# Kernel tuning notes

Hardware: AMD Instinct MI355X
Metric: run time of the kernel (lower is better)

The kernel has to match this reference:

```python
import jax, jax.numpy as jnp
import numpy as np

SQRT2PI = float(np.sqrt(2.0 * np.pi))
DN = 20          # disperse_number / heat-map side
OUT_CH = 32      # conv out_channels
MINY, MAXY, SD = 0.0, 50.0, 0.3
BN_EPS = 1e-5


def setup_inputs() -> dict:
    key = jax.random.key(0)
    ks = jax.random.split(key, 8)
    N_ATOM, N_ELE, N_NODE = 65536, 16384, 8192
    oe = jax.random.uniform(ks[0], (N_ATOM, 17), dtype=jnp.float32)
    node_ele_idx = jax.random.randint(ks[1], (N_ELE, 4), 0, N_ATOM, dtype=jnp.int64)
    ele_atom_idx = jax.random.randint(ks[2], (N_NODE, 2), 0, N_ELE, dtype=jnp.int64)
    conv_w = jax.random.normal(ks[3], (OUT_CH, 1, 3, 3), dtype=jnp.float32) * 0.1
    conv_b = jnp.zeros((OUT_CH,), jnp.float32)
    bn_gamma = jnp.ones((OUT_CH,), jnp.float32)
    bn_beta = jnp.zeros((OUT_CH,), jnp.float32)
    w1 = jax.random.normal(ks[4], (500, OUT_CH * DN * DN), dtype=jnp.float32) * 0.01
    b1 = jnp.zeros((500,), jnp.float32)
    w2 = jax.random.normal(ks[5], (60, 500), dtype=jnp.float32) * 0.05
    b2 = jnp.zeros((60,), jnp.float32)
    return dict(oe=oe, node_ele_idx=node_ele_idx, ele_atom_idx=ele_atom_idx,
                conv_w=conv_w, conv_b=conv_b, bn_gamma=bn_gamma, bn_beta=bn_beta,
                w1=w1, b1=b1, w2=w2, b2=b2)


def _distribute(rows):
    # rows: (N_node, 17). Gaussian soft histogram onto DN-point grid per row,
    # per-value max-normalization, masked sum over the 17 values, row max-normalization.
    grid = jnp.linspace(MINY, MAXY, DN).astype(rows.dtype)          # (DN,)
    mask = (rows > 0.0) & (rows < 110.0)                            # filter 0 < y < 110
    pdf = jnp.exp(-(grid[None, None, :] - rows[:, :, None]) ** 2 /
                  (2.0 * SD * SD)) / (SQRT2PI * SD)                 # (N, 17, DN)
    m = jnp.max(pdf, axis=-1, keepdims=True)
    pdf = jnp.where(m != 0, pdf / m, pdf)                           # yi / max(yi)
    pdf = pdf * mask[:, :, None]
    s = jnp.sum(pdf, axis=1)                                        # (N, DN)
    smax = jnp.max(s, axis=-1, keepdims=True)
    return jnp.where(smax != 0, s / smax, s)


def reference(oe, node_ele_idx, ele_atom_idx, conv_w, conv_b,
              bn_gamma, bn_beta, w1, b1, w2, b2):
    # merge_idx(oe, node_ele_idx): gather atoms per element, mean-reduce
    g = jnp.mean(oe[node_ele_idx], axis=1)                          # (N_ele, 17)
    g = g / jnp.linalg.norm(g, axis=1, keepdims=True)
    # merge_idx(..., ele_atom_idx, method='sum')
    h = jnp.sum(g[ele_atom_idx], axis=1)                            # (N_node, 17)
    d = _distribute(h)                                              # (N_node, DN)
    # outer-sum heat map: a[n,i,j] = d[n,j], b[n,i,j] = d[n,i]
    x1 = (d[:, None, :] + d[:, :, None])[:, None, :, :]             # (N_node,1,DN,DN)
    x = jax.lax.conv_general_dilated(
        x1, conv_w, window_strides=(1, 1), padding='SAME',
        dimension_numbers=('NCHW', 'OIHW', 'NCHW')) + conv_b[None, :, None, None]
    # Dropout2d is identity in eval mode. BatchNorm2d: training-mode batch stats.
    mu = jnp.mean(x, axis=(0, 2, 3), keepdims=True)
    var = jnp.var(x, axis=(0, 2, 3), keepdims=True)
    xn = (x - mu) / jnp.sqrt(var + BN_EPS)
    x = xn * bn_gamma[None, :, None, None] + bn_beta[None, :, None, None] + x1
    x = x.reshape(x.shape[0], -1)                                   # (N_node, 32*400)
    x = jax.nn.relu(x @ w1.T + b1)
    x = x @ w2.T + b2
    return x.reshape(x.shape[0], 20, 3)
```

## Files before the change

### kernel.cpp

```cpp
#include <hip/hip_runtime.h>
#include <hip/hip_bf16.h>
#include <math.h>

#define NFEAT 17
#define DN 20
#define OCH 32
#define H1 500
#define H2 60

#define DK 4

#define NPB 256
#define NBW 64

#define OFF_D      0
#define OFF_MOMP   32768
#define OFF_MT     33664
#define OFF_PLAIN  34112
#define OFF_M      36112
#define OFF_RS     100112
#define OFF_U4     116112
#define OFF_CST    118112
#define OFF_W2T    118624

__global__ __launch_bounds__(512) void k_main(const float* __restrict__ oe,
                                              const int* __restrict__ nei,
                                              const int* __restrict__ eai,
                                              const float* __restrict__ w2,
                                              const float* __restrict__ convw,
                                              const float* __restrict__ w1,
                                              float* __restrict__ dmat,
                                              float* __restrict__ momp,
                                              float* __restrict__ w2t,
                                              float* __restrict__ MT,
                                              float* __restrict__ plainU,
                                              float* __restrict__ Mmat,
                                              float* __restrict__ rowsum,
                                              int n_node) {
  __shared__ float smem[19136];
  int tid = threadIdx.x;
  int nbd = (n_node + NPB - 1) / NPB;
  int bx = blockIdx.x;

  if (bx < H1) {
    float* sW    = smem;
    float* rowRS = sW + 13440;
    float* rowRW = rowRS + 640;
    float* colCS = rowRW + 1920;
    float* colCW = colCS + 640;
    float* swq   = colCW + 1920;
    float* swp   = swq + 288;
    if (tid < OCH) {
      int c = tid;
      float w[3][3];
#pragma unroll
      for (int p = 0; p < 3; ++p)
#pragma unroll
        for (int q = 0; q < 3; ++q) w[p][q] = convw[c * 9 + p * 3 + q];
#pragma unroll
      for (int p = 0; p < 3; ++p) {
        swq[(c * 3 + p) * 3 + 0] = w[p][1] + w[p][2];
        swq[(c * 3 + p) * 3 + 1] = w[p][0] + w[p][1] + w[p][2];
        swq[(c * 3 + p) * 3 + 2] = w[p][0] + w[p][1];
      }
#pragma unroll
      for (int q = 0; q < 3; ++q) {
        swp[(c * 3 + q) * 3 + 0] = w[1][q] + w[2][q];
        swp[(c * 3 + q) * 3 + 1] = w[0][q] + w[1][q] + w[2][q];
        swp[(c * 3 + q) * 3 + 2] = w[0][q] + w[1][q];
      }
    }
    __syncthreads();

    const float* wbase = w1 + (size_t)bx * (OCH * DN * DN);
    for (int pair = tid; pair < OCH * DN; pair += 512) {
      int c = pair / DN;
      const float4* r = (const float4*)(wbase + pair * DN);
      float4 v0 = r[0], v1 = r[1], v2 = r[2], v3 = r[3], v4 = r[4];
      float first = v0.x, last = v4.w;
      float rs = v0.x + v0.y + v0.z + v0.w + v1.x + v1.y + v1.z + v1.w +
                 v2.x + v2.y + v2.z + v2.w + v3.x + v3.y + v3.z + v3.w +
                 v4.x + v4.y + v4.z + v4.w;
      float mid = rs - first - last;
#pragma unroll
      for (int p = 0; p < 3; ++p)
        rowRW[p * 640 + pair] = first * swq[(c * 3 + p) * 3 + 0] +
                                mid   * swq[(c * 3 + p) * 3 + 1] +
                                last  * swq[(c * 3 + p) * 3 + 2];
      rowRS[pair] = rs;
      float* dst = &sW[pair * 21];
      dst[0] = v0.x; dst[1] = v0.y; dst[2] = v0.z; dst[3] = v0.w;
      dst[4] = v1.x; dst[5] = v1.y; dst[6] = v1.z; dst[7] = v1.w;
      dst[8] = v2.x; dst[9] = v2.y; dst[10] = v2.z; dst[11] = v2.w;
      dst[12] = v3.x; dst[13] = v3.y; dst[14] = v3.z; dst[15] = v3.w;
      dst[16] = v4.x; dst[17] = v4.y; dst[18] = v4.z; dst[19] = v4.w;
    }
    __syncthreads();
    for (int pair = tid; pair < OCH * DN; pair += 512) {
      int c = pair / DN, j = pair - c * DN;
      const float* src = &sW[c * DN * 21 + j];
      float cs = 0.f, first = 0.f, last = 0.f;
#pragma unroll
      for (int i = 0; i < DN; ++i) {
        float vv = src[i * 21];
        cs += vv;
        if (i == 0) first = vv;
        if (i == DN - 1) last = vv;
      }
      float mid = cs - first - last;
#pragma unroll
      for (int q = 0; q < 3; ++q)
        colCW[q * 640 + pair] = first * swp[(c * 3 + q) * 3 + 0] +
                                mid   * swp[(c * 3 + q) * 3 + 1] +
                                last  * swp[(c * 3 + q) * 3 + 2];
      colCS[pair] = cs;
    }
    __syncthreads();
    if (tid < 128) {
      int c = tid >> 2, a = tid & 3;
      float m = rowRW[640 + c * 20 + a] + colCW[640 + c * 20 + a]
              + rowRW[c * 20 + a + 1]   + colCW[c * 20 + a + 1];
      if (a > 0) m += rowRW[1280 + c * 20 + a - 1] + colCW[1280 + c * 20 + a - 1];
      Mmat[((size_t)bx * OCH + c) * 4 + a] = m;
    } else if (tid >= 128 && tid < 128 + OCH) {
      int c = tid - 128;
      float s = 0.f;
#pragma unroll
      for (int i = 0; i < DN; ++i) s += rowRS[c * 20 + i];
      rowsum[(size_t)bx * OCH + c] = s;
    } else if (tid >= 192 && tid < 192 + DK) {
      int a = tid - 192;
      float s = 0.f;
#pragma unroll
      for (int c = 0; c < OCH; ++c) s += rowRS[c * 20 + a] + colCS[c * 20 + a];
      plainU[bx * DK + a] = s;
    }
    return;
  }

  int rb = bx - H1;
  if (rb < nbd) {
    float* dls = smem;
    int nl = tid >> 1, half = tid & 1;
    int n = rb * NPB + nl;

    float v[NFEAT];
#pragma unroll
    for (int f = 0; f < NFEAT; ++f) v[f] = 0.f;
    if (n < n_node) {
      int e = eai[(size_t)n * 2 + half];
      float a4[NFEAT];
#pragma unroll
      for (int f = 0; f < NFEAT; ++f) a4[f] = 0.f;
#pragma unroll
      for (int m = 0; m < 4; ++m) {
        int at = nei[(size_t)e * 4 + m];
        const float* row = oe + (size_t)at * NFEAT;
#pragma unroll
        for (int f = 0; f < NFEAT; ++f) a4[f] += row[f];
      }
      float nrm = 0.f;
#pragma unroll
      for (int f = 0; f < NFEAT; ++f) { float t = a4[f] * 0.25f; a4[f] = t; nrm += t * t; }
      float inv = 1.0f / sqrtf(nrm);
#pragma unroll
      for (int f = 0; f < NFEAT; ++f) v[f] = a4[f] * inv;
    }
    float h[NFEAT];
#pragma unroll
    for (int f = 0; f < NFEAT; ++f) h[f] = v[f] + __shfl_xor(v[f], 1);

    const float step = 50.0f / 19.0f;
    const float inv2 = 1.0f / (2.0f * 0.3f * 0.3f);
    float s0 = 0.f, s1 = 0.f, s2 = 0.f, s3 = 0.f;
    int f0 = half ? 9 : 0, f1 = half ? NFEAT : 9;
    for (int f = f0; f < f1; ++f) {
      float y = h[f];
      if (!(y > 0.0f && y < 110.0f)) continue;
      float t0 = -y, t1 = step - y, t2 = 2.f * step - y, t3 = 3.f * step - y;
      float e0 = __expf(-t0 * t0 * inv2);
      float e1 = __expf(-t1 * t1 * inv2);
      float e2 = __expf(-t2 * t2 * inv2);
      float e3 = __expf(-t3 * t3 * inv2);
      float mx = fmaxf(fmaxf(e0, e1), fmaxf(e2, e3));
      if (mx > 0.f) {
        float im = 1.0f / mx;
        s0 += e0 * im; s1 += e1 * im; s2 += e2 * im; s3 += e3 * im;
      }
    }
    s0 += __shfl_xor(s0, 1); s1 += __shfl_xor(s1, 1);
    s2 += __shfl_xor(s2, 1); s3 += __shfl_xor(s3, 1);
    float smax = fmaxf(fmaxf(s0, s1), fmaxf(s2, s3));
    float ism = (smax > 0.f) ? 1.0f / smax : 1.0f;
    if (half == 0) {
      float d0 = s0 * ism, d1 = s1 * ism, d2 = s2 * ism, d3 = s3 * ism;
      dls[nl * 5 + 0] = d0; dls[nl * 5 + 1] = d1;
      dls[nl * 5 + 2] = d2; dls[nl * 5 + 3] = d3;
      if (n < n_node)
        *(float4*)(dmat + (size_t)n * DK) = make_float4(d0, d1, d2, d3);
    }
    __syncthreads();
    if (tid < 14) {
      int u = tid;
      float acc = 0.f;
      if (u < 10) {
        int aa = 0, rem = u;
        while (rem >= DK - aa) { rem -= DK - aa; ++aa; }
        int bb = aa + rem;
        for (int l = 0; l < NPB; ++l) acc += dls[l * 5 + aa] * dls[l * 5 + bb];
      } else {
        int aa = u - 10;
        for (int l = 0; l < NPB; ++l) acc += dls[l * 5 + aa];
      }
      momp[(size_t)u * NBW + rb] = acc;
    }
    return;
  }

  int tb = rb - nbd;
  if (tb < 8) {
    float (*sT)[61] = (float(*)[61])smem;
    int o0 = tb * 64;
    int lo = tid & 63, jr = tid >> 6;
    for (int j = jr; j < H2; j += 8)
      if (o0 + lo < H1) sT[lo][j] = w2[(size_t)j * H1 + o0 + lo];
    __syncthreads();
    int jj = tid & 63, orr = tid >> 6;
    for (int ol = orr; ol < 64; ol += 8) {
      int o = o0 + ol;
      if (o < H1) w2t[(size_t)o * 64 + jj] = (jj < H2) ? sT[ol][jj] : 0.f;
    }
    return;
  }

  {
    float* swqL = smem;
    float* swpL = smem + 288;
    float* MTs  = smem + 576;
    if (tid < OCH) {
      int c = tid;
      float w[3][3];
#pragma unroll
      for (int p = 0; p < 3; ++p)
#pragma unroll
        for (int q = 0; q < 3; ++q) w[p][q] = convw[c * 9 + p * 3 + q];
#pragma unroll
      for (int p = 0; p < 3; ++p) {
        swqL[(c * 3 + p) * 3 + 0] = w[p][1] + w[p][2];
        swqL[(c * 3 + p) * 3 + 1] = w[p][0] + w[p][1] + w[p][2];
        swqL[(c * 3 + p) * 3 + 2] = w[p][0] + w[p][1];
      }
#pragma unroll
      for (int q = 0; q < 3; ++q) {
        swpL[(c * 3 + q) * 3 + 0] = w[1][q] + w[2][q];
        swpL[(c * 3 + q) * 3 + 1] = w[0][q] + w[1][q] + w[2][q];
        swpL[(c * 3 + q) * 3 + 2] = w[0][q] + w[1][q];
      }
    }
    for (int idx = tid; idx < OCH * 14; idx += 512) MTs[idx] = 0.f;
    __syncthreads();
    int c = tid & 31, grp = tid >> 5;
    float wqr[3][3], wpr[3][3];
#pragma unroll
    for (int p = 0; p < 3; ++p)
#pragma unroll
      for (int k = 0; k < 3; ++k) {
        wqr[p][k] = swqL[(c * 3 + p) * 3 + k];
        wpr[p][k] = swpL[(c * 3 + p) * 3 + k];
      }
    float T0 = 0, T1 = 0, T2 = 0, T3 = 0;
    float M0 = 0, M1 = 0, M2 = 0, M3 = 0, M4 = 0, M5 = 0, M6 = 0, M7 = 0, M8 = 0, M9 = 0;
    for (int pos = grp; pos < DN * DN; pos += 16) {
      int i = pos / DN, j = pos - (pos / DN) * DN;
      int icls = (i == 0) ? 0 : ((i == DN - 1) ? 2 : 1);
      int jcls = (j == 0) ? 0 : ((j == DN - 1) ? 2 : 1);
      float t0 = 0, t1 = 0, t2 = 0, t3 = 0;
      int p;
      p = 0 - i + 1; if ((unsigned)p <= 2u) t0 += wqr[p][jcls];
      p = 1 - i + 1; if ((unsigned)p <= 2u) t1 += wqr[p][jcls];
      p = 2 - i + 1; if ((unsigned)p <= 2u) t2 += wqr[p][jcls];
      p = 3 - i + 1; if ((unsigned)p <= 2u) t3 += wqr[p][jcls];
      p = 0 - j + 1; if ((unsigned)p <= 2u) t0 += wpr[p][icls];
      p = 1 - j + 1; if ((unsigned)p <= 2u) t1 += wpr[p][icls];
      p = 2 - j + 1; if ((unsigned)p <= 2u) t2 += wpr[p][icls];
      p = 3 - j + 1; if ((unsigned)p <= 2u) t3 += wpr[p][icls];
      T0 += t0; T1 += t1; T2 += t2; T3 += t3;
      M0 += t0 * t0; M1 += t0 * t1; M2 += t0 * t2; M3 += t0 * t3;
      M4 += t1 * t1; M5 += t1 * t2; M6 += t1 * t3;
      M7 += t2 * t2; M8 += t2 * t3; M9 += t3 * t3;
    }
    atomicAdd(&MTs[c * 14 + 0], T0); atomicAdd(&MTs[c * 14 + 1], T1);
    atomicAdd(&MTs[c * 14 + 2], T2); atomicAdd(&MTs[c * 14 + 3], T3);
    atomicAdd(&MTs[c * 14 + 4], M0); atomicAdd(&MTs[c * 14 + 5], M1);
    atomicAdd(&MTs[c * 14 + 6], M2); atomicAdd(&MTs[c * 14 + 7], M3);
    atomicAdd(&MTs[c * 14 + 8], M4); atomicAdd(&MTs[c * 14 + 9], M5);
    atomicAdd(&MTs[c * 14 + 10], M6); atomicAdd(&MTs[c * 14 + 11], M7);
    atomicAdd(&MTs[c * 14 + 12], M8); atomicAdd(&MTs[c * 14 + 13], M9);
    __syncthreads();
    for (int idx = tid; idx < OCH * 14; idx += 512) MT[idx] = MTs[idx];
  }
}

__global__ __launch_bounds__(512) void k_combine(const float* __restrict__ momp,
                                                 const float* __restrict__ MT,
                                                 const float* __restrict__ convb,
                                                 const float* __restrict__ gamma,
                                                 const float* __restrict__ beta,
                                                 const float* __restrict__ b1,
                                                 const float* __restrict__ plainU,
                                                 const float* __restrict__ Mmat,
                                                 const float* __restrict__ rowsum,
                                                 int nbd, int n_node,
                                                 float* __restrict__ U4,
                                                 float* __restrict__ Cst) {
  __shared__ float sac[OCH], scc[OCH], phat[10], S4[4], mred[14];
  int tid = threadIdx.x;
  if (tid < 14) {
    float acc = 0.f;
    const float* mp = momp + (size_t)tid * NBW;
    for (int b = 0; b < nbd; ++b) acc += mp[b];
    mred[tid] = acc;
  }
  __syncthreads();
  if (tid < 14) {
    float vv = mred[tid];
    if (tid < 10) {
      int aa = 0, rem = tid;
      while (rem >= DK - aa) { rem -= DK - aa; ++aa; }
      int bb = aa + rem;
      phat[tid] = (aa == bb ? 1.f : 2.f) * vv;
    } else {
      S4[tid - 10] = vv;
    }
  }
  __syncthreads();
  if (tid < OCH) {
    int c = tid;
    const float* mt = MT + c * 14;
    float q2 = mt[0] * S4[0] + mt[1] * S4[1] + mt[2] * S4[2] + mt[3] * S4[3];
    float q1 = 0.f;
#pragma unroll
    for (int u = 0; u < 10; ++u) q1 += mt[4 + u] * phat[u];
    float b_c = convb[c];
    float Nt = (float)n_node * 400.f;
    float S1 = q2 + Nt * b_c;
    float S2 = q1 + 2.f * b_c * q2 + Nt * b_c * b_c;
    float mu = S1 / Nt;
    float var = S2 / Nt - mu * mu;
    float aa = gamma[c] / sqrtf(var + 1e-5f);
    sac[c] = aa;
    scc[c] = aa * (b_c - mu) + beta[c];
  }
  __syncthreads();

  int o0 = blockIdx.x * 63;
  for (int idx = tid; idx < 63 * DK; idx += 512) {
    int ol = idx >> 2, a = idx & 3;
    int o = o0 + ol;
    if (o < H1) {
      float u = plainU[o * DK + a];
      const float* mrow = Mmat + (size_t)o * (OCH * 4) + a;
#pragma unroll
      for (int c = 0; c < OCH; ++c) u += sac[c] * mrow[c * 4];
      U4[o * DK + a] = u;
    }
  }
  if (tid < 63) {
    int o = o0 + tid;
    if (o < H1) {
      float s = b1[o];
      const float* rr = rowsum + (size_t)o * OCH;
#pragma unroll
      for (int c = 0; c < OCH; ++c) s += scc[c] * rr[c];
      Cst[o] = s;
    }
  }
}

#define NTN 16
__global__ __launch_bounds__(256, 4) void k_final(const float* __restrict__ dmat,
                                                  const float* __restrict__ U4,
                                                  const float* __restrict__ Cst,
                                                  const float* __restrict__ w2t,
                                                  const float* __restrict__ b2,
                                                  float* __restrict__ out, int n_node) {
  __shared__ float h1s[H1][20];
  __shared__ float pacc[4][NTN][64];
  int tid = threadIdx.x;
  int n0 = blockIdx.x * NTN;

  {
    int node = tid & 15, kq = tid >> 4;
    float4 d4 = make_float4(0.f, 0.f, 0.f, 0.f);
    if (n0 + node < n_node)
      d4 = *(const float4*)(dmat + (size_t)(n0 + node) * DK);
    for (int k = kq; k < H1; k += 16) {
      float4 u4 = *(const float4*)(U4 + (size_t)k * DK);
      float z = Cst[k] + u4.x * d4.x + u4.y * d4.y + u4.z * d4.z + u4.w * d4.w;
      h1s[k][node] = fmaxf(z, 0.f);
    }
  }
  __syncthreads();

  {
    int w = tid >> 6;
    int lane = tid & 63;
    int q = lane >> 4;
    int og = lane & 15;
    float a0x = 0.f, a0y = 0.f, a0z = 0.f, a0w = 0.f;
    float a1x = 0.f, a1y = 0.f, a1z = 0.f, a1w = 0.f;
    float a2x = 0.f, a2y = 0.f, a2z = 0.f, a2w = 0.f;
    float a3x = 0.f, a3y = 0.f, a3z = 0.f, a3w = 0.f;
    int k0 = w * 125, k1 = k0 + 125;
    for (int k = k0; k < k1; ++k) {
      float4 hv = *(const float4*)&h1s[k][q * 4];
      float4 wv = *(const float4*)(w2t + (size_t)k * 64 + og * 4);
      a0x += hv.x * wv.x; a0y += hv.x * wv.y; a0z += hv.x * wv.z; a0w += hv.x * wv.w;
      a1x += hv.y * wv.x; a1y += hv.y * wv.y; a1z += hv.y * wv.z; a1w += hv.y * wv.w;
      a2x += hv.z * wv.x; a2y += hv.z * wv.y; a2z += hv.z * wv.z; a2w += hv.z * wv.w;
      a3x += hv.w * wv.x; a3y += hv.w * wv.y; a3z += hv.w * wv.z; a3w += hv.w * wv.w;
    }
    *(float4*)&pacc[w][q * 4 + 0][og * 4] = make_float4(a0x, a0y, a0z, a0w);
    *(float4*)&pacc[w][q * 4 + 1][og * 4] = make_float4(a1x, a1y, a1z, a1w);
    *(float4*)&pacc[w][q * 4 + 2][og * 4] = make_float4(a2x, a2y, a2z, a2w);
    *(float4*)&pacc[w][q * 4 + 3][og * 4] = make_float4(a3x, a3y, a3z, a3w);
  }
  __syncthreads();

  for (int idx = tid; idx < NTN * H2; idx += 256) {
    int n = idx / H2, o = idx - n * H2;
    float vv = pacc[0][n][o] + pacc[1][n][o] + pacc[2][n][o] + pacc[3][n][o] + b2[o];
    if (n0 + n < n_node) out[(size_t)(n0 + n) * H2 + o] = vv;
  }
}

extern "C" void kernel_launch(void* const* d_in, const int* in_sizes, int n_in,
                              void* d_out, int out_size, void* d_ws, size_t ws_size,
                              hipStream_t stream) {
  const float* oe    = (const float*)d_in[0];
  const int*   nei   = (const int*)d_in[1];
  const int*   eai   = (const int*)d_in[2];
  const float* convw = (const float*)d_in[3];
  const float* convb = (const float*)d_in[4];
  const float* gamma = (const float*)d_in[5];
  const float* beta  = (const float*)d_in[6];
  const float* w1    = (const float*)d_in[7];
  const float* b1    = (const float*)d_in[8];
  const float* w2    = (const float*)d_in[9];
  const float* b2    = (const float*)d_in[10];
  float* out = (float*)d_out;
  float* ws  = (float*)d_ws;

  int n_node = in_sizes[2] / 2;

  float* dmat   = ws + OFF_D;
  float* momp   = ws + OFF_MOMP;
  float* MT     = ws + OFF_MT;
  float* plainU = ws + OFF_PLAIN;
  float* Mmat   = ws + OFF_M;
  float* rowsum = ws + OFF_RS;
  float* U4     = ws + OFF_U4;
  float* Cst    = ws + OFF_CST;
  float* w2t    = ws + OFF_W2T;

  int nbd = (n_node + NPB - 1) / NPB;
  k_main<<<H1 + nbd + 9, 512, 0, stream>>>(oe, nei, eai, w2, convw, w1,
                                           dmat, momp, w2t, MT,
                                           plainU, Mmat, rowsum, n_node);
  k_combine<<<8, 512, 0, stream>>>(momp, MT, convb, gamma, beta, b1,
                                   plainU, Mmat, rowsum, nbd, n_node, U4, Cst);
  k_final<<<(n_node + NTN - 1) / NTN, 256, 0, stream>>>(dmat, U4, Cst, w2t, b2, out, n_node);
}
```

Baseline: 51.07 us.

## Split w1 preprocessing blocks by channel half and restructure final GEMM mapping

Each w1 output row is now handled by two blocks that each cover 16 channels, which halves shared memory per block and doubles the block count. The intent is higher occupancy and more parallelism for the bandwidth-bound w1 reduction. The per-half plain sums are stored separately and added together in the combine kernel. Separately, the final 500->60 layer now uses a node-major h1 layout and gives each thread one node and 16 outputs, which changes the shared-memory and global access pattern.

```diff
diff --git a/kernel.cpp b/kernel.cpp
--- a/kernel.cpp
+++ b/kernel.cpp
@@ -17,11 +17,11 @@
 #define OFF_MOMP   32768
 #define OFF_MT     33664
 #define OFF_PLAIN  34112
-#define OFF_M      36112
-#define OFF_RS     100112
-#define OFF_U4     116112
-#define OFF_CST    118112
-#define OFF_W2T    118624
+#define OFF_M      38112
+#define OFF_RS     102112
+#define OFF_U4     118112
+#define OFF_CST    120112
+#define OFF_W2T    120624
 
 __global__ __launch_bounds__(512) void k_main(const float* __restrict__ oe,
                                               const int* __restrict__ nei,
@@ -33,22 +33,23 @@
                                               float* __restrict__ momp,
                                               float* __restrict__ w2t,
                                               float* __restrict__ MT,
-                                              float* __restrict__ plainU,
+                                              float* __restrict__ plainU2,
                                               float* __restrict__ Mmat,
                                               float* __restrict__ rowsum,
                                               int n_node) {
-  __shared__ float smem[19136];
+  __shared__ float smem[9856];
   int tid = threadIdx.x;
   int nbd = (n_node + NPB - 1) / NPB;
   int bx = blockIdx.x;
 
-  if (bx < H1) {
+  if (bx < 2 * H1) {
+    int o = bx >> 1, chalf = bx & 1, ch0 = chalf * 16;
     float* sW    = smem;
-    float* rowRS = sW + 13440;
-    float* rowRW = rowRS + 640;
-    float* colCS = rowRW + 1920;
-    float* colCW = colCS + 640;
-    float* swq   = colCW + 1920;
+    float* rowRS = sW + 6720;
+    float* rowRW = rowRS + 320;
+    float* colCS = rowRW + 960;
+    float* colCW = colCS + 320;
+    float* swq   = colCW + 960;
     float* swp   = swq + 288;
     if (tid < OCH) {
       int c = tid;
@@ -72,9 +73,11 @@
     }
     __syncthreads();
 
-    const float* wbase = w1 + (size_t)bx * (OCH * DN * DN);
-    for (int pair = tid; pair < OCH * DN; pair += 512) {
-      int c = pair / DN;
+    const float* wbase = w1 + (size_t)o * (OCH * DN * DN) + ch0 * (DN * DN);
+    if (tid < 320) {
+      int pair = tid;
+      int cl = pair / DN;
+      int c = ch0 + cl;
       const float4* r = (const float4*)(wbase + pair * DN);
       float4 v0 = r[0], v1 = r[1], v2 = r[2], v3 = r[3], v4 = r[4];
       float first = v0.x, last = v4.w;
@@ -84,7 +87,7 @@
       float mid = rs - first - last;
 #pragma unroll
       for (int p = 0; p < 3; ++p)
-        rowRW[p * 640 + pair] = first * swq[(c * 3 + p) * 3 + 0] +
+        rowRW[p * 320 + pair] = first * swq[(c * 3 + p) * 3 + 0] +
                                 mid   * swq[(c * 3 + p) * 3 + 1] +
                                 last  * swq[(c * 3 + p) * 3 + 2];
       rowRS[pair] = rs;
@@ -96,9 +99,11 @@
       dst[16] = v4.x; dst[17] = v4.y; dst[18] = v4.z; dst[19] = v4.w;
     }
     __syncthreads();
-    for (int pair = tid; pair < OCH * DN; pair += 512) {
-      int c = pair / DN, j = pair - c * DN;
-      const float* src = &sW[c * DN * 21 + j];
+    if (tid < 320) {
+      int pair = tid;
+      int cl = pair / DN, j = pair - cl * DN;
+      int c = ch0 + cl;
+      const float* src = &sW[cl * 420 + j];
       float cs = 0.f, first = 0.f, last = 0.f;
 #pragma unroll
       for (int i = 0; i < DN; ++i) {
@@ -110,35 +115,35 @@
       float mid = cs - first - last;
 #pragma unroll
       for (int q = 0; q < 3; ++q)
-        colCW[q * 640 + pair] = first * swp[(c * 3 + q) * 3 + 0] +
+        colCW[q * 320 + pair] = first * swp[(c * 3 + q) * 3 + 0] +
                                 mid   * swp[(c * 3 + q) * 3 + 1] +
                                 last  * swp[(c * 3 + q) * 3 + 2];
       colCS[pair] = cs;
     }
     __syncthreads();
-    if (tid < 128) {
-      int c = tid >> 2, a = tid & 3;
-      float m = rowRW[640 + c * 20 + a] + colCW[640 + c * 20 + a]
-              + rowRW[c * 20 + a + 1]   + colCW[c * 20 + a + 1];
-      if (a > 0) m += rowRW[1280 + c * 20 + a - 1] + colCW[1280 + c * 20 + a - 1];
-      Mmat[((size_t)bx * OCH + c) * 4 + a] = m;
-    } else if (tid >= 128 && tid < 128 + OCH) {
-      int c = tid - 128;
+    if (tid < 64) {
+      int cl = tid >> 2, a = tid & 3;
+      float m = rowRW[320 + cl * 20 + a] + colCW[320 + cl * 20 + a]
+              + rowRW[cl * 20 + a + 1]   + colCW[cl * 20 + a + 1];
+      if (a > 0) m += rowRW[640 + cl * 20 + a - 1] + colCW[640 + cl * 20 + a - 1];
+      Mmat[((size_t)o * OCH + ch0 + cl) * 4 + a] = m;
+    } else if (tid >= 64 && tid < 80) {
+      int cl = tid - 64;
       float s = 0.f;
 #pragma unroll
-      for (int i = 0; i < DN; ++i) s += rowRS[c * 20 + i];
-      rowsum[(size_t)bx * OCH + c] = s;
-    } else if (tid >= 192 && tid < 192 + DK) {
-      int a = tid - 192;
+      for (int i = 0; i < DN; ++i) s += rowRS[cl * 20 + i];
+      rowsum[(size_t)o * OCH + ch0 + cl] = s;
+    } else if (tid >= 96 && tid < 96 + DK) {
+      int a = tid - 96;
       float s = 0.f;
 #pragma unroll
-      for (int c = 0; c < OCH; ++c) s += rowRS[c * 20 + a] + colCS[c * 20 + a];
-      plainU[bx * DK + a] = s;
+      for (int cl = 0; cl < 16; ++cl) s += rowRS[cl * 20 + a] + colCS[cl * 20 + a];
+      plainU2[((size_t)o * 2 + chalf) * 4 + a] = s;
     }
     return;
   }
 
-  int rb = bx - H1;
+  int rb = bx - 2 * H1;
   if (rb < nbd) {
     float* dls = smem;
     int nl = tid >> 1, half = tid & 1;
@@ -307,7 +312,7 @@
                                                  const float* __restrict__ gamma,
                                                  const float* __restrict__ beta,
                                                  const float* __restrict__ b1,
-                                                 const float* __restrict__ plainU,
+                                                 const float* __restrict__ plainU2,
                                                  const float* __restrict__ Mmat,
                                                  const float* __restrict__ rowsum,
                                                  int nbd, int n_node,
@@ -358,7 +363,7 @@
     int ol = idx >> 2, a = idx & 3;
     int o = o0 + ol;
     if (o < H1) {
-      float u = plainU[o * DK + a];
+      float u = plainU2[((size_t)o * 2 + 0) * 4 + a] + plainU2[((size_t)o * 2 + 1) * 4 + a];
       const float* mrow = Mmat + (size_t)o * (OCH * 4) + a;
 #pragma unroll
       for (int c = 0; c < OCH; ++c) u += sac[c] * mrow[c * 4];
@@ -384,7 +389,7 @@
                                                   const float* __restrict__ w2t,
                                                   const float* __restrict__ b2,
                                                   float* __restrict__ out, int n_node) {
-  __shared__ float h1s[H1][20];
+  __shared__ float h1s2[NTN][508];
   __shared__ float pacc[4][NTN][64];
   int tid = threadIdx.x;
   int n0 = blockIdx.x * NTN;
@@ -397,33 +402,61 @@
     for (int k = kq; k < H1; k += 16) {
       float4 u4 = *(const float4*)(U4 + (size_t)k * DK);
       float z = Cst[k] + u4.x * d4.x + u4.y * d4.y + u4.z * d4.z + u4.w * d4.w;
-      h1s[k][node] = fmaxf(z, 0.f);
+      h1s2[node][k] = fmaxf(z, 0.f);
     }
   }
   __syncthreads();
 
   {
-    int w = tid >> 6;
-    int lane = tid & 63;
-    int q = lane >> 4;
-    int og = lane & 15;
-    float a0x = 0.f, a0y = 0.f, a0z = 0.f, a0w = 0.f;
-    float a1x = 0.f, a1y = 0.f, a1z = 0.f, a1w = 0.f;
-    float a2x = 0.f, a2y = 0.f, a2z = 0.f, a2w = 0.f;
-    float a3x = 0.f, a3y = 0.f, a3z = 0.f, a3w = 0.f;
-    int k0 = w * 125, k1 = k0 + 125;
-    for (int k = k0; k < k1; ++k) {
-      float4 hv = *(const float4*)&h1s[k][q * 4];
-      float4 wv = *(const float4*)(w2t + (size_t)k * 64 + og * 4);
-      a0x += hv.x * wv.x; a0y += hv.x * wv.y; a0z += hv.x * wv.z; a0w += hv.x * wv.w;
-      a1x += hv.y * wv.x; a1y += hv.y * wv.y; a1z += hv.y * wv.z; a1w += hv.y * wv.w;
-      a2x += hv.z * wv.x; a2y += hv.z * wv.y; a2z += hv.z * wv.z; a2w += hv.z * wv.w;
-      a3x += hv.w * wv.x; a3y += hv.w * wv.y; a3z += hv.w * wv.z; a3w += hv.w * wv.w;
-    }
-    *(float4*)&pacc[w][q * 4 + 0][og * 4] = make_float4(a0x, a0y, a0z, a0w);
-    *(float4*)&pacc[w][q * 4 + 1][og * 4] = make_float4(a1x, a1y, a1z, a1w);
-    *(float4*)&pacc[w][q * 4 + 2][og * 4] = make_float4(a2x, a2y, a2z, a2w);
-    *(float4*)&pacc[w][q * 4 + 3][og * 4] = make_float4(a3x, a3y, a3z, a3w);
+    int node = tid & 15, og = (tid >> 4) & 3, w = tid >> 6;
+    float acc[16];
+#pragma unroll
+    for (int i = 0; i < 16; ++i) acc[i] = 0.f;
+    for (int c = w; c < 125; c += 4) {
+      int k0 = c * 4;
+      float4 hv = *(const float4*)&h1s2[node][k0];
+      const float* wr = w2t + (size_t)k0 * 64 + og * 16;
+      {
+        const float4* w4 = (const float4*)(wr);
+        float4 b0 = w4[0], b1v = w4[1], b2v = w4[2], b3 = w4[3];
+        float hj = hv.x;
+        acc[0] += hj * b0.x;  acc[1] += hj * b0.y;  acc[2] += hj * b0.z;  acc[3] += hj * b0.w;
+        acc[4] += hj * b1v.x; acc[5] += hj * b1v.y; acc[6] += hj * b1v.z; acc[7] += hj * b1v.w;
+        acc[8] += hj * b2v.x; acc[9] += hj * b2v.y; acc[10] += hj * b2v.z; acc[11] += hj * b2v.w;
+        acc[12] += hj * b3.x; acc[13] += hj * b3.y; acc[14] += hj * b3.z; acc[15] += hj * b3.w;
+      }
+      {
+        const float4* w4 = (const float4*)(wr + 64);
+        float4 b0 = w4[0], b1v = w4[1], b2v = w4[2], b3 = w4[3];
+        float hj = hv.y;
+        acc[0] += hj * b0.x;  acc[1] += hj * b0.y;  acc[2] += hj * b0.z;  acc[3] += hj * b0.w;
+        acc[4] += hj * b1v.x; acc[5] += hj * b1v.y; acc[6] += hj * b1v.z; acc[7] += hj * b1v.w;
+        acc[8] += hj * b2v.x; acc[9] += hj * b2v.y; acc[10] += hj * b2v.z; acc[11] += hj * b2v.w;
+        acc[12] += hj * b3.x; acc[13] += hj * b3.y; acc[14] += hj * b3.z; acc[15] += hj * b3.w;
+      }
+      {
+        const float4* w4 = (const float4*)(wr + 128);
+        float4 b0 = w4[0], b1v = w4[1], b2v = w4[2], b3 = w4[3];
+        float hj = hv.z;
+        acc[0] += hj * b0.x;  acc[1] += hj * b0.y;  acc[2] += hj * b0.z;  acc[3] += hj * b0.w;
+        acc[4] += hj * b1v.x; acc[5] += hj * b1v.y; acc[6] += hj * b1v.z; acc[7] += hj * b1v.w;
+        acc[8] += hj * b2v.x; acc[9] += hj * b2v.y; acc[10] += hj * b2v.z; acc[11] += hj * b2v.w;
+        acc[12] += hj * b3.x; acc[13] += hj * b3.y; acc[14] += hj * b3.z; acc[15] += hj * b3.w;
+      }
+      {
+        const float4* w4 = (const float4*)(wr + 192);
+        float4 b0 = w4[0], b1v = w4[1], b2v = w4[2], b3 = w4[3];
+        float hj = hv.w;
+        acc[0] += hj * b0.x;  acc[1] += hj * b0.y;  acc[2] += hj * b0.z;  acc[3] += hj * b0.w;
+        acc[4] += hj * b1v.x; acc[5] += hj * b1v.y; acc[6] += hj * b1v.z; acc[7] += hj * b1v.w;
+        acc[8] += hj * b2v.x; acc[9] += hj * b2v.y; acc[10] += hj * b2v.z; acc[11] += hj * b2v.w;
+        acc[12] += hj * b3.x; acc[13] += hj * b3.y; acc[14] += hj * b3.z; acc[15] += hj * b3.w;
+      }
+    }
+#pragma unroll
+    for (int i = 0; i < 4; ++i)
+      *(float4*)&pacc[w][node][og * 16 + i * 4] =
+          make_float4(acc[i * 4 + 0], acc[i * 4 + 1], acc[i * 4 + 2], acc[i * 4 + 3]);
   }
   __syncthreads();
 
@@ -453,21 +486,21 @@
 
   int n_node = in_sizes[2] / 2;
 
-  float* dmat   = ws + OFF_D;
-  float* momp   = ws + OFF_MOMP;
-  float* MT     = ws + OFF_MT;
-  float* plainU = ws + OFF_PLAIN;
-  float* Mmat   = ws + OFF_M;
-  float* rowsum = ws + OFF_RS;
-  float* U4     = ws + OFF_U4;
-  float* Cst    = ws + OFF_CST;
-  float* w2t    = ws + OFF_W2T;
+  float* dmat    = ws + OFF_D;
+  float* momp    = ws + OFF_MOMP;
+  float* MT      = ws + OFF_MT;
+  float* plainU2 = ws + OFF_PLAIN;
+  float* Mmat    = ws + OFF_M;
+  float* rowsum  = ws + OFF_RS;
+  float* U4      = ws + OFF_U4;
+  float* Cst     = ws + OFF_CST;
+  float* w2t     = ws + OFF_W2T;
 
   int nbd = (n_node + NPB - 1) / NPB;
-  k_main<<<H1 + nbd + 9, 512, 0, stream>>>(oe, nei, eai, w2, convw, w1,
-                                           dmat, momp, w2t, MT,
-                                           plainU, Mmat, rowsum, n_node);
+  k_main<<<2 * H1 + nbd + 9, 512, 0, stream>>>(oe, nei, eai, w2, convw, w1,
+                                               dmat, momp, w2t, MT,
+                                               plainU2, Mmat, rowsum, n_node);
   k_combine<<<8, 512, 0, stream>>>(momp, MT, convb, gamma, beta, b1,
-                                   plainU, Mmat, rowsum, nbd, n_node, U4, Cst);
+                                   plainU2, Mmat, rowsum, nbd, n_node, U4, Cst);
   k_final<<<(n_node + NTN - 1) / NTN, 256, 0, stream>>>(dmat, U4, Cst, w2t, b2, out, n_node);
 }
```

After: 68.98 us. 35.1% more time.

## Fold BN-combine stage into final kernel, recomputing U4/Cst per block

Applied to the files above, without the earlier changes.

Removes the separate small combine kernel launch. Every final-kernel block now reduces the BN moments and computes its own copy of the effective layer-1 coefficients (U4) and constants (Cst) in shared memory. This saves one launch and its serialization gap, but each of the 512 blocks redundantly reads Mmat and rowsum (about 80 KB) and does the 500x32 reduction. It also adds about 10 KB of shared memory per block, which may reduce occupancy.

```diff
diff --git a/kernel.cpp b/kernel.cpp
--- a/kernel.cpp
+++ b/kernel.cpp
@@ -19,9 +19,7 @@
 #define OFF_PLAIN  34112
 #define OFF_M      36112
 #define OFF_RS     100112
-#define OFF_U4     116112
-#define OFF_CST    118112
-#define OFF_W2T    118624
+#define OFF_W2T    116112
 
 __global__ __launch_bounds__(512) void k_main(const float* __restrict__ oe,
                                               const int* __restrict__ nei,
@@ -301,36 +299,40 @@
   }
 }
 
-__global__ __launch_bounds__(512) void k_combine(const float* __restrict__ momp,
-                                                 const float* __restrict__ MT,
-                                                 const float* __restrict__ convb,
-                                                 const float* __restrict__ gamma,
-                                                 const float* __restrict__ beta,
-                                                 const float* __restrict__ b1,
-                                                 const float* __restrict__ plainU,
-                                                 const float* __restrict__ Mmat,
-                                                 const float* __restrict__ rowsum,
-                                                 int nbd, int n_node,
-                                                 float* __restrict__ U4,
-                                                 float* __restrict__ Cst) {
-  __shared__ float sac[OCH], scc[OCH], phat[10], S4[4], mred[14];
+#define NTN 16
+__global__ __launch_bounds__(256, 4) void k_final(const float* __restrict__ dmat,
+                                                  const float* __restrict__ momp,
+                                                  const float* __restrict__ MT,
+                                                  const float* __restrict__ convb,
+                                                  const float* __restrict__ gamma,
+                                                  const float* __restrict__ beta,
+                                                  const float* __restrict__ b1,
+                                                  const float* __restrict__ plainU,
+                                                  const float* __restrict__ Mmat,
+                                                  const float* __restrict__ rowsum,
+                                                  const float* __restrict__ w2t,
+                                                  const float* __restrict__ b2,
+                                                  float* __restrict__ out,
+                                                  int nbd, int n_node) {
+  __shared__ float h1s[H1][20];
+  __shared__ float pacc[4][NTN][64];
+  __shared__ float u4s[H1][4];
+  __shared__ float cstL[512];
+  __shared__ float sac[OCH], scc[OCH], phat[10], S4[4];
   int tid = threadIdx.x;
+  int n0 = blockIdx.x * NTN;
+
   if (tid < 14) {
     float acc = 0.f;
     const float* mp = momp + (size_t)tid * NBW;
     for (int b = 0; b < nbd; ++b) acc += mp[b];
-    mred[tid] = acc;
-  }
-  __syncthreads();
-  if (tid < 14) {
-    float vv = mred[tid];
     if (tid < 10) {
       int aa = 0, rem = tid;
       while (rem >= DK - aa) { rem -= DK - aa; ++aa; }
       int bb = aa + rem;
-      phat[tid] = (aa == bb ? 1.f : 2.f) * vv;
+      phat[tid] = (aa == bb ? 1.f : 2.f) * acc;
     } else {
-      S4[tid - 10] = vv;
+      S4[tid - 10] = acc;
     }
   }
   __syncthreads();
@@ -352,42 +354,27 @@
     scc[c] = aa * (b_c - mu) + beta[c];
   }
   __syncthreads();
-
-  int o0 = blockIdx.x * 63;
-  for (int idx = tid; idx < 63 * DK; idx += 512) {
-    int ol = idx >> 2, a = idx & 3;
-    int o = o0 + ol;
-    if (o < H1) {
-      float u = plainU[o * DK + a];
-      const float* mrow = Mmat + (size_t)o * (OCH * 4) + a;
-#pragma unroll
-      for (int c = 0; c < OCH; ++c) u += sac[c] * mrow[c * 4];
-      U4[o * DK + a] = u;
-    }
-  }
-  if (tid < 63) {
-    int o = o0 + tid;
-    if (o < H1) {
-      float s = b1[o];
-      const float* rr = rowsum + (size_t)o * OCH;
-#pragma unroll
-      for (int c = 0; c < OCH; ++c) s += scc[c] * rr[c];
-      Cst[o] = s;
-    }
-  }
-}
-
-#define NTN 16
-__global__ __launch_bounds__(256, 4) void k_final(const float* __restrict__ dmat,
-                                                  const float* __restrict__ U4,
-                                                  const float* __restrict__ Cst,
-                                                  const float* __restrict__ w2t,
-                                                  const float* __restrict__ b2,
-                                                  float* __restrict__ out, int n_node) {
-  __shared__ float h1s[H1][20];
-  __shared__ float pacc[4][NTN][64];
-  int tid = threadIdx.x;
-  int n0 = blockIdx.x * NTN;
+  {
+    float sacr[OCH], sccr[OCH];
+#pragma unroll
+    for (int c = 0; c < OCH; ++c) { sacr[c] = sac[c]; sccr[c] = scc[c]; }
+    for (int k = tid; k < H1; k += 256) {
+      float4 u = *(const float4*)(plainU + k * DK);
+      const float4* mr = (const float4*)(Mmat + (size_t)k * (OCH * 4));
+      const float* rr = rowsum + (size_t)k * OCH;
+      float s = b1[k];
+#pragma unroll
+      for (int c = 0; c < OCH; ++c) {
+        float4 m = mr[c];
+        float a = sacr[c];
+        u.x += a * m.x; u.y += a * m.y; u.z += a * m.z; u.w += a * m.w;
+        s += sccr[c] * rr[c];
+      }
+      *(float4*)&u4s[k][0] = u;
+      cstL[k] = s;
+    }
+  }
+  __syncthreads();
 
   {
     int node = tid & 15, kq = tid >> 4;
@@ -395,8 +382,8 @@
     if (n0 + node < n_node)
       d4 = *(const float4*)(dmat + (size_t)(n0 + node) * DK);
     for (int k = kq; k < H1; k += 16) {
-      float4 u4 = *(const float4*)(U4 + (size_t)k * DK);
-      float z = Cst[k] + u4.x * d4.x + u4.y * d4.y + u4.z * d4.z + u4.w * d4.w;
+      float4 u4 = *(const float4*)&u4s[k][0];
+      float z = cstL[k] + u4.x * d4.x + u4.y * d4.y + u4.z * d4.z + u4.w * d4.w;
       h1s[k][node] = fmaxf(z, 0.f);
     }
   }
@@ -459,15 +446,14 @@
   float* plainU = ws + OFF_PLAIN;
   float* Mmat   = ws + OFF_M;
   float* rowsum = ws + OFF_RS;
-  float* U4     = ws + OFF_U4;
-  float* Cst    = ws + OFF_CST;
   float* w2t    = ws + OFF_W2T;
 
   int nbd = (n_node + NPB - 1) / NPB;
   k_main<<<H1 + nbd + 9, 512, 0, stream>>>(oe, nei, eai, w2, convw, w1,
                                            dmat, momp, w2t, MT,
                                            plainU, Mmat, rowsum, n_node);
-  k_combine<<<8, 512, 0, stream>>>(momp, MT, convb, gamma, beta, b1,
-                                   plainU, Mmat, rowsum, nbd, n_node, U4, Cst);
-  k_final<<<(n_node + NTN - 1) / NTN, 256, 0, stream>>>(dmat, U4, Cst, w2t, b2, out, n_node);
+  k_final<<<(n_node + NTN - 1) / NTN, 256, 0, stream>>>(dmat, momp, MT, convb,
+                                                        gamma, beta, b1, plainU,
+                                                        Mmat, rowsum, w2t, b2,
+                                                        out, nbd, n_node);
 }
```

Result: slower. 73.43 us (+43.8%).
